# Optimization experiments

Hardware: AMD Instinct MI355X
Metric: run time of the kernel (lower is better)

The kernel has to match this reference:

```python
import jax, jax.numpy as jnp
import numpy as np
import math

PATCHES = [(2, 2), (4, 4), (8, 8), (16, 16)]  # (width, height) per scale
D_MODEL = 256
EPS = 1e-5


def setup_inputs() -> dict:
    key = jax.random.key(0)
    ks = jax.random.split(key, 12)
    b, c, h, w = 4, D_MODEL, 128, 128
    s = 1.0 / math.sqrt(c)
    inp = {
        'x': jax.random.normal(ks[0], (b, c, h, w), jnp.float32),
        'y': jax.random.normal(ks[1], (b, c, h, w), jnp.float32),
        'Wq': jax.random.normal(ks[2], (c, c), jnp.float32) * s,
        'bq': jnp.zeros((c,), jnp.float32),
        'Wk': jax.random.normal(ks[3], (c, c), jnp.float32) * s,
        'bk': jnp.zeros((c,), jnp.float32),
        'Wv': jax.random.normal(ks[4], (c, c), jnp.float32) * s,
        'bv': jnp.zeros((c,), jnp.float32),
        'Wo': jax.random.normal(ks[5], (c, c, 3, 3), jnp.float32) * (1.0 / math.sqrt(c * 9)),
        'bo': jnp.zeros((c,), jnp.float32),
        'gamma': jnp.ones((c,), jnp.float32),
        'beta': jnp.zeros((c,), jnp.float32),
    }
    return inp


def _conv1x1(x, W, b):
    # 1x1 conv == channel matmul
    return jnp.einsum('oc,bchw->bohw', W, x) + b[None, :, None, None]


def _windowed_attention(q, k, v, ww, hh):
    # q,k,v: [b, d_k, h, w] -> windows of (hh, ww), tokens = out_h*out_w
    b, d_k, h, w = q.shape
    out_h, out_w = h // hh, w // ww

    def to_tokens(t):
        t = t.reshape(b, d_k, out_h, hh, out_w, ww)
        t = t.transpose(0, 2, 4, 1, 3, 5)  # b, out_h, out_w, d_k, hh, ww
        return t.reshape(b, out_h * out_w, d_k * hh * ww)

    qt, kt, vt = to_tokens(q), to_tokens(k), to_tokens(v)
    scale = 1.0 / math.sqrt(qt.shape[-1])
    scores = jnp.einsum('bnd,bmd->bnm', qt, kt) * scale
    p = jax.nn.softmax(scores, axis=-1)
    out = jnp.einsum('bnm,bmd->bnd', p, vt)
    out = out.reshape(b, out_h, out_w, d_k, hh, ww)
    out = out.transpose(0, 3, 1, 4, 2, 5).reshape(b, d_k, h, w)
    return out


def reference(x, y, Wq, bq, Wk, bk, Wv, bv, Wo, bo, gamma, beta):
    b, c, h, w = x.shape
    n_scales = len(PATCHES)
    d_k = c // n_scales

    q_all = _conv1x1(x, Wq, bq)
    k_all = _conv1x1(y, Wk, bk)
    v_all = _conv1x1(y, Wv, bv)

    outs = []
    for i, (ww, hh) in enumerate(PATCHES):
        sl = slice(i * d_k, (i + 1) * d_k)
        outs.append(_windowed_attention(q_all[:, sl], k_all[:, sl], v_all[:, sl], ww, hh))
    out = jnp.concatenate(outs, axis=1)  # [b, c, h, w]

    # output_linear: Conv3x3 (pad 1) -> BatchNorm2d (batch stats) -> LeakyReLU(0.2)
    z = jax.lax.conv_general_dilated(
        out, Wo, window_strides=(1, 1), padding='SAME',
        dimension_numbers=('NCHW', 'OIHW', 'NCHW')) + bo[None, :, None, None]
    mean = jnp.mean(z, axis=(0, 2, 3), keepdims=True)
    var = jnp.var(z, axis=(0, 2, 3), keepdims=True)
    zn = (z - mean) * jax.lax.rsqrt(var + EPS)
    zn = zn * gamma[None, :, None, None] + beta[None, :, None, None]
    return jnp.where(zn >= 0, zn, 0.2 * zn)
```

## Files before the change

### kernel.cpp

```cpp
#include <hip/hip_runtime.h>
#include <math.h>

#define BN 4
#define CC 256
#define HH_ 128
#define WW_ 128
#define HWP (HH_*WW_)
#define TOK (64*HWP)


typedef __attribute__((ext_vector_type(8))) short bf16x8;
typedef __attribute__((ext_vector_type(4))) float f32x4;

__device__ __forceinline__ float bf2f(unsigned short u) {
    return __uint_as_float(((unsigned)u) << 16);
}
__device__ __forceinline__ unsigned short f2bf(float f) {
    unsigned u = __float_as_uint(f);
    u += 0x7FFF + ((u >> 16) & 1);
    return (unsigned short)(u >> 16);
}
__device__ __forceinline__ void load4f(const unsigned short* p, float o[4]) {
    ushort4 v = *(const ushort4*)p;
    o[0] = bf2f(v.x); o[1] = bf2f(v.y); o[2] = bf2f(v.z); o[3] = bf2f(v.w);
}
__device__ __forceinline__ float ld1(const unsigned short* p) { return bf2f(*p); }
__device__ __forceinline__ float ld1(const float* p) { return *p; }
__device__ __forceinline__ void st1(unsigned short* p, float v) { *p = f2bf(v); }
__device__ __forceinline__ void st1(float* p, float v) { *p = v; }

__device__ __forceinline__ void gload16(const void* g, void* l) {
    __builtin_amdgcn_global_load_lds(
        (__attribute__((address_space(1))) void*)(g),
        (__attribute__((address_space(3))) void*)(l), 16, 0, 0);
}

__device__ __forceinline__ void stage64(
    const unsigned short* src, size_t strideElems, unsigned short* lds, int t)
{
    #pragma unroll
    for (int k = 0; k < 4; k++) {
        int n = t + k * 256;
        int row = n >> 3, slot = n & 7;
        const char* gp = (const char*)(src + (size_t)row * strideElems)
                       + ((slot ^ (row & 7)) << 4);
        gload16(gp, (char*)lds + n * 16);
    }
}

__device__ __forceinline__ void mfma_iter_swz(
    const unsigned short* As, const unsigned short* Bs,
    int wm, int wn, int lr, int quad, f32x4 acc[4][4])
{
    #pragma unroll
    for (int s = 0; s < 2; s++) {
        bf16x8 af[4], bfr[4];
        #pragma unroll
        for (int i = 0; i < 4; i++) {
            int row = wm*64 + i*16 + lr;
            int off = (row << 7) + (s << 6) + (quad << 4);
            af[i] = *(const bf16x8*)((const char*)As + (off ^ ((row & 7) << 4)));
        }
        #pragma unroll
        for (int j = 0; j < 4; j++) {
            int row = wn*64 + j*16 + lr;
            int off = (row << 7) + (s << 6) + (quad << 4);
            bfr[j] = *(const bf16x8*)((const char*)Bs + (off ^ ((row & 7) << 4)));
        }
        #pragma unroll
        for (int i = 0; i < 4; i++)
            #pragma unroll
            for (int j = 0; j < 4; j++)
                acc[i][j] = __builtin_amdgcn_mfma_f32_16x16x32_bf16(
                    af[i], bfr[j], acc[i][j], 0, 0, 0);
    }
}

#define LDS_STRIDE 72

struct Tile32 { uint4 v[4]; };

__device__ __forceinline__ Tile32 load_tile_bf16(
    const unsigned short* src, size_t stride, int t)
{
    int r = t >> 1, kc = (t & 1) * 32;
    const uint4* sp = (const uint4*)(src + (size_t)r * stride + kc);
    Tile32 o;
    o.v[0] = sp[0]; o.v[1] = sp[1]; o.v[2] = sp[2]; o.v[3] = sp[3];
    return o;
}

__device__ __forceinline__ void store_tile(
    unsigned short* lds, const Tile32& d, int t)
{
    int r = t >> 1, kc = (t & 1) * 32;
    uint4* dp = (uint4*)&lds[r * LDS_STRIDE + kc];
    dp[0] = d.v[0]; dp[1] = d.v[1]; dp[2] = d.v[2]; dp[3] = d.v[3];
}

__device__ __forceinline__ void mfma_iter(
    const unsigned short* As, const unsigned short* Bs,
    int wm, int wn, int lr, int quad, f32x4 acc[4][4])
{
    #pragma unroll
    for (int s = 0; s < 2; s++) {
        bf16x8 af[4], bfr[4];
        #pragma unroll
        for (int i = 0; i < 4; i++)
            af[i] = *(const bf16x8*)&As[(wm*64 + i*16 + lr) * LDS_STRIDE + s*32 + quad*8];
        #pragma unroll
        for (int j = 0; j < 4; j++)
            bfr[j] = *(const bf16x8*)&Bs[(wn*64 + j*16 + lr) * LDS_STRIDE + s*32 + quad*8];
        #pragma unroll
        for (int i = 0; i < 4; i++)
            #pragma unroll
            for (int j = 0; j < 4; j++)
                acc[i][j] = __builtin_amdgcn_mfma_f32_16x16x32_bf16(
                    af[i], bfr[j], acc[i][j], 0, 0, 0);
    }
}

__global__ __launch_bounds__(256) void zero_kernel(float* __restrict__ p)
{
    p[blockIdx.x * 256 + threadIdx.x] = 0.f;
}

__global__ __launch_bounds__(256) void nchw_to_nhwc(
    const float* __restrict__ x, const float* __restrict__ y,
    unsigned short* __restrict__ xt, unsigned short* __restrict__ yt)
{
    __shared__ unsigned short T[64 * 72];
    int z = blockIdx.z;
    int b = z & 3, which = z >> 2;
    const float* src = (which ? y : x) + (size_t)b * CC * HWP;
    unsigned short* dst = (which ? yt : xt) + (size_t)b * HWP * CC;
    int p0 = blockIdx.x * 64, c0 = blockIdx.y * 64;
    int t = threadIdx.x;

    int cl = t >> 2, pc = (t & 3) * 16;
    #pragma unroll
    for (int e = 0; e < 16; e += 4) {
        float4 v = *(const float4*)&src[(size_t)(c0 + cl) * HWP + p0 + pc + e];
        T[(pc + e + 0) * 72 + cl] = f2bf(v.x);
        T[(pc + e + 1) * 72 + cl] = f2bf(v.y);
        T[(pc + e + 2) * 72 + cl] = f2bf(v.z);
        T[(pc + e + 3) * 72 + cl] = f2bf(v.w);
    }
    __syncthreads();
    int p = t >> 2, cc = (t & 3) * 16;
    uint4 a = *(uint4*)&T[p * 72 + cc];
    uint4 bsec = *(uint4*)&T[p * 72 + cc + 8];
    uint4* dp = (uint4*)&dst[(size_t)(p0 + p) * CC + c0 + cc];
    dp[0] = a; dp[1] = bsec;
}

__global__ __launch_bounds__(256) void wpack_kernel(
    const float* __restrict__ Wo, unsigned short* __restrict__ wpack)
{
    int o = blockIdx.x, c = threadIdx.x;
    const float* wr = Wo + ((size_t)o * CC + c) * 9;
    #pragma unroll
    for (int tap = 0; tap < 9; tap++)
        wpack[((size_t)o * 9 + tap) * CC + c] = f2bf(wr[tap]);
}

__global__ __launch_bounds__(256) void wqkv_pack(
    const float* __restrict__ Wq, const float* __restrict__ Wk,
    const float* __restrict__ Wv, unsigned short* __restrict__ Wb)
{
    int which = blockIdx.x;
    const float* W = which == 0 ? Wq : (which == 1 ? Wk : Wv);
    unsigned short* o = Wb + (size_t)which * 65536;
    for (int i = threadIdx.x; i < 65536; i += 256)
        o[i] = f2bf(W[i]);
}

__global__ __launch_bounds__(256) void proj_gemm(
    const unsigned short* __restrict__ xt, const unsigned short* __restrict__ yt,
    const unsigned short* __restrict__ Wqkv,
    const float* __restrict__ bq, const float* __restrict__ bk,
    const float* __restrict__ bv,
    unsigned short* __restrict__ qt, unsigned short* __restrict__ kt,
    unsigned short* __restrict__ vt)
{
    __shared__ unsigned short Asb[2][8192], Bsb[2][8192];
    int z = blockIdx.z, b = z & 3, which = z >> 2;
    const unsigned short* src = (which == 0) ? xt : yt;
    const float* bias = (which == 0) ? bq : (which == 1 ? bk : bv);
    unsigned short* outp = (which == 0) ? qt : (which == 1 ? kt : vt);

    int m0 = blockIdx.y * 128;
    int n0 = blockIdx.x * 128;
    const unsigned short* A = Wqkv + (size_t)which * 65536 + (size_t)m0 * CC;
    const unsigned short* B = src + ((size_t)b * HWP + n0) * CC;

    int t = threadIdx.x, w = t >> 6, lane = t & 63;
    int quad = lane >> 4, lr = lane & 15, wm = w >> 1, wn = w & 1;

    f32x4 acc[4][4];
    #pragma unroll
    for (int i = 0; i < 4; i++)
        #pragma unroll
        for (int j = 0; j < 4; j++) acc[i][j] = (f32x4){0.f, 0.f, 0.f, 0.f};

    stage64(A, CC, Asb[0], t);
    stage64(B, CC, Bsb[0], t);
    __syncthreads();
    int cur = 0;
    for (int k0 = 0; k0 < CC; k0 += 64) {
        if (k0 + 64 < CC) {
            stage64(A + k0 + 64, CC, Asb[cur ^ 1], t);
            stage64(B + k0 + 64, CC, Bsb[cur ^ 1], t);
        }
        mfma_iter_swz(Asb[cur], Bsb[cur], wm, wn, lr, quad, acc);
        __syncthreads();
        cur ^= 1;
    }

    #pragma unroll
    for (int i = 0; i < 4; i++) {
        int obase = m0 + wm * 64 + i * 16 + quad * 4;
        #pragma unroll
        for (int rr = 0; rr < 4; rr++) {
            int o = obase + rr;
            int s = o >> 6, lg = s + 1;
            int ch = o & 63;
            float bia = bias[o];
            unsigned short* ob = outp + ((size_t)s * 4 + b) * TOK;
            #pragma unroll
            for (int j = 0; j < 4; j++) {
                int p = n0 + wn * 64 + j * 16 + lr;
                int yy = p >> 7, xx = p & 127;
                int oy = yy >> lg, wy = yy & ((1 << lg) - 1);
                int ox = xx >> lg, wx = xx & ((1 << lg) - 1);
                int tokn = (oy << (7 - lg)) + ox;
                int didx = (ch << (2 * lg)) + (wy << lg) + wx;
                size_t idx;
                if (which == 2 && s < 3)
                    idx = ((size_t)didx << (14 - 2 * lg)) + tokn;
                else
                    idx = ((size_t)tokn << (6 + 2 * lg)) + didx;
                ob[idx] = f2bf(acc[i][j][rr] + bia);
            }
        }
    }
}

#define PS_STRIDE 136

__global__ __launch_bounds__(512) void flash0(
    const unsigned short* __restrict__ qt, const unsigned short* __restrict__ kt,
    const unsigned short* __restrict__ vt, float* __restrict__ part,
    float* __restrict__ rs0g)
{
    __shared__ unsigned short Ps[64 * PS_STRIDE];
    __shared__ unsigned short Bs[256 * 64];

    int L = blockIdx.x;
    int xcd = L & 7, slot = L >> 3;
    int b = xcd >> 1;
    int idx = slot + 64 * (xcd & 1);
    int h = idx >> 6;
    int q0 = (idx & 63) * 64;
    int kvbase = h * 2048;

    const unsigned short* Qb = qt + (size_t)b * TOK;
    const unsigned short* Kb = kt + (size_t)b * TOK;
    const unsigned short* Vb = vt + (size_t)b * TOK;

    int t = threadIdx.x, w = t >> 6, lane = t & 63;
    int quad = lane >> 4, lr = lane & 15;
    int wm = w >> 2, wn = w & 3;

    bf16x8 aq[4][2][2];
    #pragma unroll
    for (int k = 0; k < 4; k++)
        #pragma unroll
        for (int s = 0; s < 2; s++)
            #pragma unroll
            for (int i = 0; i < 2; i++)
                aq[k][s][i] = *(const bf16x8*)&Qb[
                    (size_t)(q0 + wm*32 + i*16 + lr) * 256 + k*64 + s*32 + quad*8];

    f32x4 acc_o[2][4];
    #pragma unroll
    for (int i = 0; i < 2; i++)
        #pragma unroll
        for (int j = 0; j < 4; j++) acc_o[i][j] = (f32x4){0.f, 0.f, 0.f, 0.f};
    float rsum[2][4] = {};

    const float SC = 1.f / 16.f;

    for (int kv0 = kvbase; kv0 < kvbase + 2048; kv0 += 128) {
        f32x4 acc_s[2][2];
        #pragma unroll
        for (int i = 0; i < 2; i++)
            #pragma unroll
            for (int j = 0; j < 2; j++) acc_s[i][j] = (f32x4){0.f, 0.f, 0.f, 0.f};

        #pragma unroll
        for (int kp = 0; kp < 2; kp++) {
            __syncthreads();
            #pragma unroll
            for (int k = 0; k < 4; k++) {
                int n = t + k * 512;
                int R = n >> 3, sl = n & 7;
                int kl = R & 127, dsub = R >> 7;
                const char* gp = (const char*)(Kb + (size_t)(kv0 + kl) * 256
                                 + kp*128 + dsub*64) + ((sl ^ (R & 7)) << 4);
                gload16(gp, (char*)Bs + n * 16);
            }
            __syncthreads();
            __builtin_amdgcn_s_setprio(1);
            #pragma unroll
            for (int t2 = 0; t2 < 2; t2++)
                #pragma unroll
                for (int s = 0; s < 2; s++) {
                    bf16x8 bfr[2];
                    #pragma unroll
                    for (int j = 0; j < 2; j++) {
                        int row = t2*128 + wn*32 + j*16 + lr;
                        int off = (row << 7) + (s << 6) + (quad << 4);
                        bfr[j] = *(const bf16x8*)((const char*)Bs
                                   + (off ^ ((row & 7) << 4)));
                    }
                    #pragma unroll
                    for (int i = 0; i < 2; i++)
                        #pragma unroll
                        for (int j = 0; j < 2; j++)
                            acc_s[i][j] = __builtin_amdgcn_mfma_f32_16x16x32_bf16(
                                aq[kp*2 + t2][s][i], bfr[j], acc_s[i][j], 0, 0, 0);
                }
            __builtin_amdgcn_s_setprio(0);
        }

        #pragma unroll
        for (int i = 0; i < 2; i++)
            #pragma unroll
            for (int j = 0; j < 2; j++)
                #pragma unroll
                for (int rr = 0; rr < 4; rr++) {
                    float e = __expf(acc_s[i][j][rr] * SC);
                    Ps[(wm*32 + i*16 + quad*4 + rr) * PS_STRIDE + wn*32 + j*16 + lr]
                        = f2bf(e);
                    rsum[i][rr] += e;
                }

        #pragma unroll
        for (int ks = 0; ks < 2; ks++) {
            __syncthreads();
            #pragma unroll
            for (int k = 0; k < 4; k++) {
                int n = t + k * 512;
                int R = n >> 3, sl = n & 7;
                const char* gp = (const char*)(Vb + (size_t)R * 4096 + kv0 + ks*64)
                               + ((sl ^ (R & 7)) << 4);
                gload16(gp, (char*)Bs + n * 16);
            }
            __syncthreads();
            __builtin_amdgcn_s_setprio(1);
            #pragma unroll
            for (int s = 0; s < 2; s++) {
                bf16x8 pa[2], vb[4];
                #pragma unroll
                for (int i = 0; i < 2; i++)
                    pa[i] = *(const bf16x8*)&Ps[
                        (wm*32 + i*16 + lr) * PS_STRIDE + ks*64 + s*32 + quad*8];
                #pragma unroll
                for (int j = 0; j < 4; j++) {
                    int row = wn*64 + j*16 + lr;
                    int off = (row << 7) + (s << 6) + (quad << 4);
                    vb[j] = *(const bf16x8*)((const char*)Bs
                              + (off ^ ((row & 7) << 4)));
                }
                #pragma unroll
                for (int i = 0; i < 2; i++)
                    #pragma unroll
                    for (int j = 0; j < 4; j++)
                        acc_o[i][j] = __builtin_amdgcn_mfma_f32_16x16x32_bf16(
                            pa[i], vb[j], acc_o[i][j], 0, 0, 0);
            }
            __builtin_amdgcn_s_setprio(0);
        }
    }

    #pragma unroll
    for (int i = 0; i < 2; i++)
        #pragma unroll
        for (int rr = 0; rr < 4; rr++) {
            float v = rsum[i][rr];
            v += __shfl_xor(v, 1); v += __shfl_xor(v, 2);
            v += __shfl_xor(v, 4); v += __shfl_xor(v, 8);
            if (lr == 0)
                atomicAdd(&rs0g[b * 4096 + q0 + wm*32 + i*16 + quad*4 + rr], v);
        }
    float* op = part + ((size_t)(h * 4 + b)) * TOK;
    #pragma unroll
    for (int i = 0; i < 2; i++)
        #pragma unroll
        for (int rr = 0; rr < 4; rr++) {
            int tokl = wm*32 + i*16 + quad*4 + rr;
            float* orow = op + (size_t)(q0 + tokl) * 256;
            #pragma unroll
            for (int j = 0; j < 4; j++)
                orow[wn*64 + j*16 + lr] = acc_o[i][j][rr];
        }
}

__global__ __launch_bounds__(256) void combine0f(
    const float* __restrict__ part, const float* __restrict__ rs,
    unsigned short* __restrict__ aot)
{
    int b = blockIdx.y;
    int tok0 = blockIdx.x * 16;
    const float* p0 = part + (size_t)b * TOK;
    const float* p1 = part + (size_t)(4 + b) * TOK;
    int t = threadIdx.x;
    int w = t >> 6, ch = t & 63;
    int wy = w >> 1, wx = w & 1;
    #pragma unroll 4
    for (int u = 0; u < 16; u++) {
        int tok = tok0 + u;
        size_t base = (size_t)tok * 256 + ch * 4 + w;
        float v = (p0[base] + p1[base]) * (1.f / rs[b * 4096 + tok]);
        int oy = tok >> 6, ox = tok & 63;
        int yy = oy * 2 + wy, xx = ox * 2 + wx;
        aot[((size_t)b * HWP + yy * WW_ + xx) * CC + ch] = f2bf(v);
    }
}

template<int NTOK, int DD>
__global__ __launch_bounds__(256) void s_gemm_exp(
    const unsigned short* __restrict__ Qb, const unsigned short* __restrict__ Kb,
    unsigned short* __restrict__ S0, float* __restrict__ rsg, float sc)
{
    __shared__ unsigned short Asb[2][8192], Bsb[2][8192];
    int bz = blockIdx.z;
    int m0 = blockIdx.y * 128, n0 = blockIdx.x * 128;
    const unsigned short* Q = Qb + (size_t)bz * TOK + (size_t)m0 * DD;
    const unsigned short* K = Kb + (size_t)bz * TOK + (size_t)n0 * DD;
    unsigned short* S = S0 + (size_t)bz * NTOK * NTOK;
    float* rs = rsg + (size_t)bz * NTOK;

    int t = threadIdx.x, w = t >> 6, lane = t & 63;
    int quad = lane >> 4, lr = lane & 15, wm = w >> 1, wn = w & 1;

    f32x4 acc[4][4];
    #pragma unroll
    for (int i = 0; i < 4; i++)
        #pragma unroll
        for (int j = 0; j < 4; j++) acc[i][j] = (f32x4){0.f, 0.f, 0.f, 0.f};

    stage64(Q, DD, Asb[0], t);
    stage64(K, DD, Bsb[0], t);
    __syncthreads();
    int cur = 0;
    for (int k0 = 0; k0 < DD; k0 += 64) {
        if (k0 + 64 < DD) {
            stage64(Q + k0 + 64, DD, Asb[cur ^ 1], t);
            stage64(K + k0 + 64, DD, Bsb[cur ^ 1], t);
        }
        mfma_iter_swz(Asb[cur], Bsb[cur], wm, wn, lr, quad, acc);
        __syncthreads();
        cur ^= 1;
    }

    #pragma unroll
    for (int i = 0; i < 4; i++) {
        int m = m0 + wm * 64 + i * 16 + quad * 4;
        float rsum[4] = {0.f, 0.f, 0.f, 0.f};
        #pragma unroll
        for (int j = 0; j < 4; j++) {
            int n = n0 + wn * 64 + j * 16 + lr;
            #pragma unroll
            for (int rr = 0; rr < 4; rr++) {
                float e = __expf(acc[i][j][rr] * sc);
                S[(size_t)(m + rr) * NTOK + n] = f2bf(e);
                rsum[rr] += e;
            }
        }
        #pragma unroll
        for (int rr = 0; rr < 4; rr++) {
            float v = rsum[rr];
            v += __shfl_xor(v, 1);
            v += __shfl_xor(v, 2);
            v += __shfl_xor(v, 4);
            v += __shfl_xor(v, 8);
            if (lr == 0) atomicAdd(&rs[m + rr], v);
        }
    }
}

template<int NTOK, int DD, int LG, int CH0>
__global__ __launch_bounds__(256) void o_gemm(
    const unsigned short* __restrict__ Pb, const unsigned short* __restrict__ Vb,
    const float* __restrict__ rsg, unsigned short* __restrict__ aot, int b0)
{
    __shared__ unsigned short Asb[2][8192], Bsb[2][8192];
    int bz = blockIdx.z, b = b0 + bz;
    int m0 = blockIdx.y * 128, n0 = blockIdx.x * 128;
    const unsigned short* P = Pb + (size_t)bz * NTOK * NTOK + (size_t)m0 * NTOK;
    const unsigned short* V = Vb + (size_t)bz * TOK + (size_t)n0 * NTOK;
    const float* rs = rsg + (size_t)bz * NTOK;

    int t = threadIdx.x, w = t >> 6, lane = t & 63;
    int quad = lane >> 4, lr = lane & 15, wm = w >> 1, wn = w & 1;

    f32x4 acc[4][4];
    #pragma unroll
    for (int i = 0; i < 4; i++)
        #pragma unroll
        for (int j = 0; j < 4; j++) acc[i][j] = (f32x4){0.f, 0.f, 0.f, 0.f};

    stage64(P, NTOK, Asb[0], t);
    stage64(V, NTOK, Bsb[0], t);
    __syncthreads();
    int cur = 0;
    for (int k0 = 0; k0 < NTOK; k0 += 64) {
        if (k0 + 64 < NTOK) {
            stage64(P + k0 + 64, NTOK, Asb[cur ^ 1], t);
            stage64(V + k0 + 64, NTOK, Bsb[cur ^ 1], t);
        }
        mfma_iter_swz(Asb[cur], Bsb[cur], wm, wn, lr, quad, acc);
        __syncthreads();
        cur ^= 1;
    }

    #pragma unroll
    for (int i = 0; i < 4; i++) {
        int tb0 = m0 + wm * 64 + i * 16 + quad * 4;
        #pragma unroll
        for (int rr = 0; rr < 4; rr++) {
            int tokn = tb0 + rr;
            float inv = 1.f / rs[tokn];
            int oy = tokn >> (7 - LG), ox = tokn & ((1 << (7 - LG)) - 1);
            #pragma unroll
            for (int j = 0; j < 4; j++) {
                int d = n0 + wn * 64 + j * 16 + lr;
                int ch = d >> (2 * LG);
                int r2 = d & ((1 << (2 * LG)) - 1);
                int wy = r2 >> LG, wx = r2 & ((1 << LG) - 1);
                int yy = (oy << LG) + wy, xx = (ox << LG) + wx;
                aot[((size_t)b * HWP + yy * WW_ + xx) * CC + CH0 + ch] =
                    f2bf(acc[i][j][rr] * inv);
            }
        }
    }
}

__global__ __launch_bounds__(256) void s2_partial(
    const unsigned short* __restrict__ Qb, const unsigned short* __restrict__ Kb,
    float* __restrict__ S2p)
{
    __shared__ unsigned short Asb[2][8192], Bsb[2][8192];
    int z = blockIdx.z, b = z >> 3, sp = z & 7;
    int m0 = blockIdx.y * 128, n0 = blockIdx.x * 128;
    const unsigned short* Q = Qb + (size_t)b * TOK + (size_t)m0 * 4096 + sp * 512;
    const unsigned short* K = Kb + (size_t)b * TOK + (size_t)n0 * 4096 + sp * 512;
    float* So = S2p + ((size_t)(sp * 4 + b)) * 65536;

    int t = threadIdx.x, w = t >> 6, lane = t & 63;
    int quad = lane >> 4, lr = lane & 15, wm = w >> 1, wn = w & 1;

    f32x4 acc[4][4];
    #pragma unroll
    for (int i = 0; i < 4; i++)
        #pragma unroll
        for (int j = 0; j < 4; j++) acc[i][j] = (f32x4){0.f, 0.f, 0.f, 0.f};

    stage64(Q, 4096, Asb[0], t);
    stage64(K, 4096, Bsb[0], t);
    __syncthreads();
    int cur = 0;
    for (int k0 = 0; k0 < 512; k0 += 64) {
        if (k0 + 64 < 512) {
            stage64(Q + k0 + 64, 4096, Asb[cur ^ 1], t);
            stage64(K + k0 + 64, 4096, Bsb[cur ^ 1], t);
        }
        mfma_iter_swz(Asb[cur], Bsb[cur], wm, wn, lr, quad, acc);
        __syncthreads();
        cur ^= 1;
    }

    #pragma unroll
    for (int i = 0; i < 4; i++) {
        int m = m0 + wm * 64 + i * 16 + quad * 4;
        #pragma unroll
        for (int j = 0; j < 4; j++) {
            int n = n0 + wn * 64 + j * 16 + lr;
            #pragma unroll
            for (int rr = 0; rr < 4; rr++)
                So[(size_t)(m + rr) * 256 + n] = acc[i][j][rr];
        }
    }
}

__global__ __launch_bounds__(256) void s2_finish(
    const float* __restrict__ S2p, unsigned short* __restrict__ Sbf,
    float* __restrict__ rs2, float sc)
{
    int row = blockIdx.x, b = blockIdx.y, t = threadIdx.x;
    float v = 0.f;
    #pragma unroll
    for (int sp = 0; sp < 8; sp++)
        v += S2p[((size_t)(sp * 4 + b)) * 65536 + row * 256 + t];
    float e = __expf(v * sc);
    Sbf[((size_t)b * 65536) + row * 256 + t] = f2bf(e);
    __shared__ float red[256];
    red[t] = e; __syncthreads();
    for (int s = 128; s > 0; s >>= 1) {
        if (t < s) red[t] += red[t + s];
        __syncthreads();
    }
    if (t == 0) rs2[b * 256 + row] = red[0];
}

__device__ __forceinline__ Tile32 load_tile_conv(
    const unsigned short* aob, int ys, int dx, int cbase, int t)
{
    int r = t >> 1, kc = (t & 1) * 32;
    int xs = r + dx;
    Tile32 o;
    if (ys >= 0 && ys < HH_ && xs >= 0 && xs < WW_) {
        const uint4* sp = (const uint4*)(aob + ((size_t)ys * WW_ + xs) * CC + cbase + kc);
        o.v[0] = sp[0]; o.v[1] = sp[1]; o.v[2] = sp[2]; o.v[3] = sp[3];
    } else {
        uint4 zz = make_uint4(0, 0, 0, 0);
        o.v[0] = zz; o.v[1] = zz; o.v[2] = zz; o.v[3] = zz;
    }
    return o;
}

__global__ __launch_bounds__(256) void conv_gemm(
    const unsigned short* __restrict__ aot, const unsigned short* __restrict__ wpack,
    const float* __restrict__ bo, float* __restrict__ zout,
    float* __restrict__ stats)
{
    __shared__ unsigned short As[128 * LDS_STRIDE], Bs[128 * LDS_STRIDE];
    int yrow = blockIdx.x;
    int o0 = blockIdx.y * 128;
    int b = blockIdx.z;
    const unsigned short* aob = aot + (size_t)b * HWP * CC;
    const unsigned short* wsrc = wpack + (size_t)o0 * 2304;

    int t = threadIdx.x, w = t >> 6, lane = t & 63;
    int quad = lane >> 4, lr = lane & 15, wm = w >> 1, wn = w & 1;

    f32x4 acc[4][4];
    #pragma unroll
    for (int i = 0; i < 4; i++)
        #pragma unroll
        for (int j = 0; j < 4; j++) acc[i][j] = (f32x4){0.f, 0.f, 0.f, 0.f};

    for (int tap = 0; tap < 9; tap++) {
        int dy = tap / 3 - 1, dx = tap % 3 - 1;
        int ys = yrow + dy;
        for (int cb = 0; cb < CC; cb += 64) {
            Tile32 ta = load_tile_bf16(wsrc + tap * CC + cb, 2304, t);
            Tile32 tb = load_tile_conv(aob, ys, dx, cb, t);
            __syncthreads();
            store_tile(As, ta, t); store_tile(Bs, tb, t);
            __syncthreads();
            mfma_iter(As, Bs, wm, wn, lr, quad, acc);
        }
    }

    #pragma unroll
    for (int i = 0; i < 4; i++) {
        #pragma unroll
        for (int rr = 0; rr < 4; rr++) {
            int o = o0 + wm * 64 + i * 16 + quad * 4 + rr;
            float bia = bo[o];
            float s1 = 0.f, s2v = 0.f;
            #pragma unroll
            for (int j = 0; j < 4; j++) {
                int x = wn * 64 + j * 16 + lr;
                float v = acc[i][j][rr] + bia;
                zout[((size_t)(b * CC + o)) * HWP + yrow * WW_ + x] = v;
                s1 += v; s2v = fmaf(v, v, s2v);
            }
            s1 += __shfl_xor(s1, 1); s2v += __shfl_xor(s2v, 1);
            s1 += __shfl_xor(s1, 2); s2v += __shfl_xor(s2v, 2);
            s1 += __shfl_xor(s1, 4); s2v += __shfl_xor(s2v, 4);
            s1 += __shfl_xor(s1, 8); s2v += __shfl_xor(s2v, 8);
            if (lr == 0) {
                atomicAdd(&stats[o], s1);
                atomicAdd(&stats[CC + o], s2v);
            }
        }
    }
}

__global__ __launch_bounds__(256) void stats_finalize(
    float* __restrict__ stats, const float* __restrict__ gamma,
    const float* __restrict__ beta)
{
    int c = threadIdx.x;
    const float inv_n = 1.f / (BN * HWP);
    float mean = stats[c] * inv_n;
    float var = stats[CC + c] * inv_n - mean * mean;
    float rstd = rsqrtf(var + 1e-5f);
    float gs = gamma[c] * rstd;
    stats[c] = gs;
    stats[CC + c] = beta[c] - mean * gs;
}

__global__ __launch_bounds__(256) void s3_kernel(
    const unsigned short* __restrict__ Qb, const unsigned short* __restrict__ Kb,
    float* __restrict__ S, float sc)
{
    const int N = 64, D = 16384, KLEN = 1024;
    int b = blockIdx.z >> 4, kc = blockIdx.z & 15;
    const unsigned short* Q = Qb + (size_t)b * TOK;
    const unsigned short* K = Kb + (size_t)b * TOK;
    float* Sb = S + (size_t)b * N * N;
    int k0 = kc * KLEN;

    __shared__ float As[16][64], Bs[16][64];
    int t = threadIdx.x, tx = t & 15, ty = t >> 4, r = t >> 2, q = t & 3;

    float acc[4][4] = {};
    for (int kk = k0; kk < k0 + KLEN; kk += 16) {
        float a4[4], b4[4];
        load4f(&Q[(size_t)r * D + kk + q * 4], a4);
        load4f(&K[(size_t)r * D + kk + q * 4], b4);
        __syncthreads();
        As[q*4+0][r] = a4[0]; As[q*4+1][r] = a4[1]; As[q*4+2][r] = a4[2]; As[q*4+3][r] = a4[3];
        Bs[q*4+0][r] = b4[0]; Bs[q*4+1][r] = b4[1]; Bs[q*4+2][r] = b4[2]; Bs[q*4+3][r] = b4[3];
        __syncthreads();
        #pragma unroll
        for (int k = 0; k < 16; k++) {
            float4 af = *(const float4*)&As[k][ty*4];
            float4 bf = *(const float4*)&Bs[k][tx*4];
            float ar[4] = {af.x, af.y, af.z, af.w};
            float br[4] = {bf.x, bf.y, bf.z, bf.w};
            #pragma unroll
            for (int ii = 0; ii < 4; ii++)
                #pragma unroll
                for (int jj = 0; jj < 4; jj++)
                    acc[ii][jj] = fmaf(ar[ii], br[jj], acc[ii][jj]);
        }
    }

    #pragma unroll
    for (int ii = 0; ii < 4; ii++)
        #pragma unroll
        for (int jj = 0; jj < 4; jj++)
            atomicAdd(&Sb[(size_t)(ty * 4 + ii) * N + tx * 4 + jj], acc[ii][jj] * sc);
}

template<typename T>
__global__ __launch_bounds__(256) void softmax_kernel(T* __restrict__ S, int n)
{
    int b = blockIdx.y;
    int row = blockIdx.x;
    T* rp = S + (size_t)b * n * n + (size_t)row * n;
    __shared__ float red[256];
    int t = threadIdx.x;

    float m = -1e30f;
    for (int j = t; j < n; j += 256) m = fmaxf(m, ld1(&rp[j]));
    red[t] = m; __syncthreads();
    for (int s = 128; s > 0; s >>= 1) { if (t < s) red[t] = fmaxf(red[t], red[t + s]); __syncthreads(); }
    m = red[0]; __syncthreads();

    float sum = 0.f;
    for (int j = t; j < n; j += 256) { float e = __expf(ld1(&rp[j]) - m); st1(&rp[j], e); sum += e; }
    red[t] = sum; __syncthreads();
    for (int s = 128; s > 0; s >>= 1) { if (t < s) red[t] += red[t + s]; __syncthreads(); }
    float inv = 1.f / red[0];
    for (int j = t; j < n; j += 256) st1(&rp[j], ld1(&rp[j]) * inv);
}

__global__ __launch_bounds__(256) void o3_kernel(
    const float* __restrict__ P, const unsigned short* __restrict__ Vb,
    unsigned short* __restrict__ aot)
{
    const int N = 64, D = 16384, LG = 4, CH0 = 192;
    int bz = blockIdx.z;
    const float* Pb = P + (size_t)bz * N * N;
    const unsigned short* V = Vb + (size_t)bz * TOK;
    int i0 = blockIdx.x * 64, d0 = blockIdx.y * 64;

    __shared__ float Ps[16][64];
    __shared__ float Vs[16][64];
    int t = threadIdx.x, tx = t & 15, ty = t >> 4, r = t >> 2, q = t & 3;
    int vr = t >> 4, vq = t & 15;

    float acc[4][4] = {};
    for (int j0 = 0; j0 < N; j0 += 16) {
        float p4[4], v4[4];
        float4 pv = *(const float4*)&Pb[(size_t)(i0 + r) * N + j0 + q * 4];
        p4[0] = pv.x; p4[1] = pv.y; p4[2] = pv.z; p4[3] = pv.w;
        load4f(&V[(size_t)(j0 + vr) * D + d0 + vq * 4], v4);
        __syncthreads();
        Ps[q*4+0][r] = p4[0]; Ps[q*4+1][r] = p4[1]; Ps[q*4+2][r] = p4[2]; Ps[q*4+3][r] = p4[3];
        Vs[vr][vq*4+0] = v4[0]; Vs[vr][vq*4+1] = v4[1]; Vs[vr][vq*4+2] = v4[2]; Vs[vr][vq*4+3] = v4[3];
        __syncthreads();
        #pragma unroll
        for (int k = 0; k < 16; k++) {
            float4 pf = *(const float4*)&Ps[k][ty*4];
            float4 vf = *(const float4*)&Vs[k][tx*4];
            float pr[4] = {pf.x, pf.y, pf.z, pf.w};
            float vrr[4] = {vf.x, vf.y, vf.z, vf.w};
            #pragma unroll
            for (int ii = 0; ii < 4; ii++)
                #pragma unroll
                for (int jj = 0; jj < 4; jj++)
                    acc[ii][jj] = fmaf(pr[ii], vrr[jj], acc[ii][jj]);
        }
    }

    #pragma unroll
    for (int ii = 0; ii < 4; ii++) {
        int tokn = i0 + ty * 4 + ii;
        int oy = tokn >> (7 - LG), ox = tokn & ((1 << (7 - LG)) - 1);
        #pragma unroll
        for (int jj = 0; jj < 4; jj++) {
            int d = d0 + tx * 4 + jj;
            int ch = d >> (2 * LG);
            int r2 = d & ((1 << (2 * LG)) - 1);
            int wy = r2 >> LG, wx = r2 & ((1 << LG) - 1);
            int yy = (oy << LG) + wy, xx = (ox << LG) + wx;
            aot[((size_t)bz * HWP + yy * WW_ + xx) * CC + CH0 + ch] = f2bf(acc[ii][jj]);
        }
    }
}

__global__ __launch_bounds__(256) void bn_apply_kernel(
    float* __restrict__ z, const float* __restrict__ stats)
{
    size_t i4 = (size_t)blockIdx.x * 256 + threadIdx.x;
    size_t idx = i4 * 4;
    int c = (int)((idx >> 14) & 255);
    float gs = stats[c], gb = stats[CC + c];
    float4 v = *(float4*)&z[idx];
    v.x = fmaf(v.x, gs, gb); v.y = fmaf(v.y, gs, gb);
    v.z = fmaf(v.z, gs, gb); v.w = fmaf(v.w, gs, gb);
    v.x = v.x >= 0.f ? v.x : 0.2f * v.x;
    v.y = v.y >= 0.f ? v.y : 0.2f * v.y;
    v.z = v.z >= 0.f ? v.z : 0.2f * v.z;
    v.w = v.w >= 0.f ? v.w : 0.2f * v.w;
    *(float4*)&z[idx] = v;
}

extern "C" void kernel_launch(void* const* d_in, const int* in_sizes, int n_in,
                              void* d_out, int out_size, void* d_ws, size_t ws_size,
                              hipStream_t stream)
{
    const float* x     = (const float*)d_in[0];
    const float* y     = (const float*)d_in[1];
    const float* Wq    = (const float*)d_in[2];
    const float* bq    = (const float*)d_in[3];
    const float* Wk    = (const float*)d_in[4];
    const float* bk    = (const float*)d_in[5];
    const float* Wv    = (const float*)d_in[6];
    const float* bv    = (const float*)d_in[7];
    const float* Wo    = (const float*)d_in[8];
    const float* bo    = (const float*)d_in[9];
    const float* gamma = (const float*)d_in[10];
    const float* beta  = (const float*)d_in[11];
    float* out = (float*)d_out;

    unsigned short* qt    = (unsigned short*)d_ws;
    unsigned short* kt    = qt + (size_t)16777216;
    unsigned short* vt    = kt + (size_t)16777216;
    unsigned short* aot   = vt + (size_t)16777216;
    unsigned short* Sbf   = aot + (size_t)16777216;
    unsigned short* wpack = Sbf + (size_t)16777216;
    float* stats = (float*)(wpack + (size_t)589824);
    float* S3    = stats + 512;
    float* rs0   = S3 + 16384;
    float* rs1   = rs0 + 16384;
    float* rs2   = rs1 + 4096;
    unsigned short* xt = Sbf;
    unsigned short* yt = aot;
    float* part = (float*)d_out;
    unsigned short* Wqkv_bf = (unsigned short*)((char*)d_out + (size_t)33554432);
    float* S2p = (float*)d_out;

    dim3 blk(256);

    zero_kernel<<<dim3(150), blk, 0, stream>>>(stats);
    nchw_to_nhwc<<<dim3(256, 4, 8), blk, 0, stream>>>(x, y, xt, yt);
    wpack_kernel<<<dim3(256), blk, 0, stream>>>(Wo, wpack);
    wqkv_pack<<<dim3(3), blk, 0, stream>>>(Wq, Wk, Wv, Wqkv_bf);

    proj_gemm<<<dim3(128, 2, 12), blk, 0, stream>>>(
        xt, yt, Wqkv_bf, bq, bk, bv, qt, kt, vt);

    flash0<<<dim3(512), dim3(512), 0, stream>>>(qt, kt, vt, part, rs0);
    combine0f<<<dim3(256, 4), blk, 0, stream>>>(part, rs0, aot);

    s_gemm_exp<1024, 1024><<<dim3(8, 8, 4), blk, 0, stream>>>(
        qt + (size_t)4 * TOK, kt + (size_t)4 * TOK, Sbf, rs1, 1.f / 32.f);
    o_gemm<1024, 1024, 2, 64><<<dim3(8, 8, 4), blk, 0, stream>>>(
        Sbf, vt + (size_t)4 * TOK, rs1, aot, 0);

    s2_partial<<<dim3(2, 2, 32), blk, 0, stream>>>(
        qt + (size_t)8 * TOK, kt + (size_t)8 * TOK, S2p);
    s2_finish<<<dim3(256, 4), blk, 0, stream>>>(S2p, Sbf, rs2, 1.f / 64.f);
    o_gemm<256, 4096, 3, 128><<<dim3(32, 2, 4), blk, 0, stream>>>(
        Sbf, vt + (size_t)8 * TOK, rs2, aot, 0);

    s3_kernel<<<dim3(1, 1, 64), blk, 0, stream>>>(
        qt + (size_t)12 * TOK, kt + (size_t)12 * TOK, S3, 1.f / 128.f);
    softmax_kernel<float><<<dim3(64, 4), blk, 0, stream>>>(S3, 64);
    o3_kernel<<<dim3(1, 256, 4), blk, 0, stream>>>(S3, vt + (size_t)12 * TOK, aot);

    conv_gemm<<<dim3(128, 2, 4), blk, 0, stream>>>(aot, wpack, bo, out, stats);
    stats_finalize<<<dim3(1), blk, 0, stream>>>(stats, gamma, beta);
    bn_apply_kernel<<<dim3(16384), blk, 0, stream>>>(out, stats);
}
```

Before: 870.5 us.

## Pad conv input, pipeline conv GEMM, move scale-3 attention to MFMA, fold BN finalize

The attention output buffer now has a one-pixel zero border, so the 3x3 conv GEMM can use async global-to-LDS double-buffered staging with swizzled MFMA reads and no bounds checks. The scale-3 score and PV kernels move from scalar FP32 FMA loops to bf16 MFMA kernels, and the V projection for scale 3 switches to a transposed layout to match. The stats finalize kernel is folded into bn_apply, and the workspace is reorganised. In exchange, an extra zero-fill pass over the padded buffer is added, and scale-3 P is rounded to bf16.

```diff
diff --git a/kernel.cpp b/kernel.cpp
--- a/kernel.cpp
+++ b/kernel.cpp
@@ -20,13 +20,7 @@
     u += 0x7FFF + ((u >> 16) & 1);
     return (unsigned short)(u >> 16);
 }
-__device__ __forceinline__ void load4f(const unsigned short* p, float o[4]) {
-    ushort4 v = *(const ushort4*)p;
-    o[0] = bf2f(v.x); o[1] = bf2f(v.y); o[2] = bf2f(v.z); o[3] = bf2f(v.w);
-}
-__device__ __forceinline__ float ld1(const unsigned short* p) { return bf2f(*p); }
 __device__ __forceinline__ float ld1(const float* p) { return *p; }
-__device__ __forceinline__ void st1(unsigned short* p, float v) { *p = f2bf(v); }
 __device__ __forceinline__ void st1(float* p, float v) { *p = v; }
 
 __device__ __forceinline__ void gload16(const void* g, void* l) {
@@ -48,6 +42,19 @@
     }
 }
 
+__device__ __forceinline__ void stage32(
+    const unsigned short* src, size_t strideElems, unsigned short* lds, int t)
+{
+    #pragma unroll
+    for (int k = 0; k < 2; k++) {
+        int n = t + k * 256;
+        int row = n >> 3, slot = n & 7;
+        const char* gp = (const char*)(src + (size_t)row * strideElems)
+                       + ((slot ^ (row & 7)) << 4);
+        gload16(gp, (char*)lds + n * 16);
+    }
+}
+
 __device__ __forceinline__ void mfma_iter_swz(
     const unsigned short* As, const unsigned short* Bs,
     int wm, int wn, int lr, int quad, f32x4 acc[4][4])
@@ -76,53 +83,16 @@
     }
 }
 
-#define LDS_STRIDE 72
-
-struct Tile32 { uint4 v[4]; };
-
-__device__ __forceinline__ Tile32 load_tile_bf16(
-    const unsigned short* src, size_t stride, int t)
-{
-    int r = t >> 1, kc = (t & 1) * 32;
-    const uint4* sp = (const uint4*)(src + (size_t)r * stride + kc);
-    Tile32 o;
-    o.v[0] = sp[0]; o.v[1] = sp[1]; o.v[2] = sp[2]; o.v[3] = sp[3];
-    return o;
-}
-
-__device__ __forceinline__ void store_tile(
-    unsigned short* lds, const Tile32& d, int t)
-{
-    int r = t >> 1, kc = (t & 1) * 32;
-    uint4* dp = (uint4*)&lds[r * LDS_STRIDE + kc];
-    dp[0] = d.v[0]; dp[1] = d.v[1]; dp[2] = d.v[2]; dp[3] = d.v[3];
-}
-
-__device__ __forceinline__ void mfma_iter(
-    const unsigned short* As, const unsigned short* Bs,
-    int wm, int wn, int lr, int quad, f32x4 acc[4][4])
-{
-    #pragma unroll
-    for (int s = 0; s < 2; s++) {
-        bf16x8 af[4], bfr[4];
-        #pragma unroll
-        for (int i = 0; i < 4; i++)
-            af[i] = *(const bf16x8*)&As[(wm*64 + i*16 + lr) * LDS_STRIDE + s*32 + quad*8];
-        #pragma unroll
-        for (int j = 0; j < 4; j++)
-            bfr[j] = *(const bf16x8*)&Bs[(wn*64 + j*16 + lr) * LDS_STRIDE + s*32 + quad*8];
-        #pragma unroll
-        for (int i = 0; i < 4; i++)
-            #pragma unroll
-            for (int j = 0; j < 4; j++)
-                acc[i][j] = __builtin_amdgcn_mfma_f32_16x16x32_bf16(
-                    af[i], bfr[j], acc[i][j], 0, 0, 0);
-    }
-}
-
 __global__ __launch_bounds__(256) void zero_kernel(float* __restrict__ p)
 {
     p[blockIdx.x * 256 + threadIdx.x] = 0.f;
+}
+
+__global__ __launch_bounds__(256) void zero4(uint4* __restrict__ p, int n4)
+{
+    uint4 z = make_uint4(0, 0, 0, 0);
+    for (int i = blockIdx.x * 256 + threadIdx.x; i < n4; i += gridDim.x * 256)
+        p[i] = z;
 }
 
 __global__ __launch_bounds__(256) void nchw_to_nhwc(
@@ -236,7 +206,7 @@
                 int tokn = (oy << (7 - lg)) + ox;
                 int didx = (ch << (2 * lg)) + (wy << lg) + wx;
                 size_t idx;
-                if (which == 2 && s < 3)
+                if (which == 2)
                     idx = ((size_t)didx << (14 - 2 * lg)) + tokn;
                 else
                     idx = ((size_t)tokn << (6 + 2 * lg)) + didx;
@@ -409,7 +379,7 @@
 
 __global__ __launch_bounds__(256) void combine0f(
     const float* __restrict__ part, const float* __restrict__ rs,
-    unsigned short* __restrict__ aot)
+    unsigned short* __restrict__ aotp)
 {
     int b = blockIdx.y;
     int tok0 = blockIdx.x * 16;
@@ -425,7 +395,7 @@
         float v = (p0[base] + p1[base]) * (1.f / rs[b * 4096 + tok]);
         int oy = tok >> 6, ox = tok & 63;
         int yy = oy * 2 + wy, xx = ox * 2 + wx;
-        aot[((size_t)b * HWP + yy * WW_ + xx) * CC + ch] = f2bf(v);
+        aotp[((size_t)(b * 130 + yy + 1) * 130 + xx + 1) * CC + ch] = f2bf(v);
     }
 }
 
@@ -494,7 +464,7 @@
 template<int NTOK, int DD, int LG, int CH0>
 __global__ __launch_bounds__(256) void o_gemm(
     const unsigned short* __restrict__ Pb, const unsigned short* __restrict__ Vb,
-    const float* __restrict__ rsg, unsigned short* __restrict__ aot, int b0)
+    const float* __restrict__ rsg, unsigned short* __restrict__ aotp, int b0)
 {
     __shared__ unsigned short Asb[2][8192], Bsb[2][8192];
     int bz = blockIdx.z, b = b0 + bz;
@@ -541,7 +511,7 @@
                 int r2 = d & ((1 << (2 * LG)) - 1);
                 int wy = r2 >> LG, wx = r2 & ((1 << LG) - 1);
                 int yy = (oy << LG) + wy, xx = (ox << LG) + wx;
-                aot[((size_t)b * HWP + yy * WW_ + xx) * CC + CH0 + ch] =
+                aotp[((size_t)(b * 130 + yy + 1) * 130 + xx + 1) * CC + CH0 + ch] =
                     f2bf(acc[i][j][rr] * inv);
             }
         }
@@ -615,32 +585,16 @@
     if (t == 0) rs2[b * 256 + row] = red[0];
 }
 
-__device__ __forceinline__ Tile32 load_tile_conv(
-    const unsigned short* aob, int ys, int dx, int cbase, int t)
-{
-    int r = t >> 1, kc = (t & 1) * 32;
-    int xs = r + dx;
-    Tile32 o;
-    if (ys >= 0 && ys < HH_ && xs >= 0 && xs < WW_) {
-        const uint4* sp = (const uint4*)(aob + ((size_t)ys * WW_ + xs) * CC + cbase + kc);
-        o.v[0] = sp[0]; o.v[1] = sp[1]; o.v[2] = sp[2]; o.v[3] = sp[3];
-    } else {
-        uint4 zz = make_uint4(0, 0, 0, 0);
-        o.v[0] = zz; o.v[1] = zz; o.v[2] = zz; o.v[3] = zz;
-    }
-    return o;
-}
-
 __global__ __launch_bounds__(256) void conv_gemm(
-    const unsigned short* __restrict__ aot, const unsigned short* __restrict__ wpack,
+    const unsigned short* __restrict__ aotp, const unsigned short* __restrict__ wpack,
     const float* __restrict__ bo, float* __restrict__ zout,
     float* __restrict__ stats)
 {
-    __shared__ unsigned short As[128 * LDS_STRIDE], Bs[128 * LDS_STRIDE];
+    __shared__ unsigned short Asb[2][8192], Bsb[2][8192];
     int yrow = blockIdx.x;
     int o0 = blockIdx.y * 128;
     int b = blockIdx.z;
-    const unsigned short* aob = aot + (size_t)b * HWP * CC;
+    const unsigned short* aob = aotp + (size_t)b * 130 * 130 * 256;
     const unsigned short* wsrc = wpack + (size_t)o0 * 2304;
 
     int t = threadIdx.x, w = t >> 6, lane = t & 63;
@@ -652,17 +606,26 @@
         #pragma unroll
         for (int j = 0; j < 4; j++) acc[i][j] = (f32x4){0.f, 0.f, 0.f, 0.f};
 
-    for (int tap = 0; tap < 9; tap++) {
-        int dy = tap / 3 - 1, dx = tap % 3 - 1;
-        int ys = yrow + dy;
-        for (int cb = 0; cb < CC; cb += 64) {
-            Tile32 ta = load_tile_bf16(wsrc + tap * CC + cb, 2304, t);
-            Tile32 tb = load_tile_conv(aob, ys, dx, cb, t);
-            __syncthreads();
-            store_tile(As, ta, t); store_tile(Bs, tb, t);
-            __syncthreads();
-            mfma_iter(As, Bs, wm, wn, lr, quad, acc);
-        }
+    stage64(wsrc, 2304, Asb[0], t);
+    {
+        int ys = yrow - 1;
+        stage64(aob + ((size_t)(ys + 1) * 130 + 0) * 256, 256, Bsb[0], t);
+    }
+    __syncthreads();
+    int cur = 0;
+    for (int kk = 0; kk < 36; kk++) {
+        if (kk + 1 < 36) {
+            int kn = kk + 1;
+            int tap = kn >> 2, cb = (kn & 3) * 64;
+            int dy = tap / 3 - 1, dx = tap % 3 - 1;
+            int ys = yrow + dy;
+            stage64(wsrc + tap * 256 + cb, 2304, Asb[cur ^ 1], t);
+            stage64(aob + ((size_t)(ys + 1) * 130 + (dx + 1)) * 256 + cb, 256,
+                    Bsb[cur ^ 1], t);
+        }
+        mfma_iter_swz(Asb[cur], Bsb[cur], wm, wn, lr, quad, acc);
+        __syncthreads();
+        cur ^= 1;
     }
 
     #pragma unroll
@@ -691,62 +654,71 @@
     }
 }
 
-__global__ __launch_bounds__(256) void stats_finalize(
-    float* __restrict__ stats, const float* __restrict__ gamma,
-    const float* __restrict__ beta)
-{
-    int c = threadIdx.x;
-    const float inv_n = 1.f / (BN * HWP);
-    float mean = stats[c] * inv_n;
-    float var = stats[CC + c] * inv_n - mean * mean;
-    float rstd = rsqrtf(var + 1e-5f);
-    float gs = gamma[c] * rstd;
-    stats[c] = gs;
-    stats[CC + c] = beta[c] - mean * gs;
-}
-
-__global__ __launch_bounds__(256) void s3_kernel(
+__global__ __launch_bounds__(256) void s3_mfma(
     const unsigned short* __restrict__ Qb, const unsigned short* __restrict__ Kb,
     float* __restrict__ S, float sc)
 {
-    const int N = 64, D = 16384, KLEN = 1024;
-    int b = blockIdx.z >> 4, kc = blockIdx.z & 15;
-    const unsigned short* Q = Qb + (size_t)b * TOK;
-    const unsigned short* K = Kb + (size_t)b * TOK;
-    float* Sb = S + (size_t)b * N * N;
-    int k0 = kc * KLEN;
-
-    __shared__ float As[16][64], Bs[16][64];
-    int t = threadIdx.x, tx = t & 15, ty = t >> 4, r = t >> 2, q = t & 3;
-
-    float acc[4][4] = {};
-    for (int kk = k0; kk < k0 + KLEN; kk += 16) {
-        float a4[4], b4[4];
-        load4f(&Q[(size_t)r * D + kk + q * 4], a4);
-        load4f(&K[(size_t)r * D + kk + q * 4], b4);
+    __shared__ unsigned short Asb[2][4096], Bsb[2][4096];
+    int z = blockIdx.x, b = z >> 4, kc = z & 15;
+    const unsigned short* Q = Qb + (size_t)b * TOK + kc * 1024;
+    const unsigned short* K = Kb + (size_t)b * TOK + kc * 1024;
+    float* Sb = S + (size_t)b * 4096;
+
+    int t = threadIdx.x, w = t >> 6, lane = t & 63;
+    int quad = lane >> 4, lr = lane & 15, wm = w >> 1, wn = w & 1;
+
+    f32x4 acc[2][2];
+    #pragma unroll
+    for (int i = 0; i < 2; i++)
+        #pragma unroll
+        for (int j = 0; j < 2; j++) acc[i][j] = (f32x4){0.f, 0.f, 0.f, 0.f};
+
+    stage32(Q, 16384, Asb[0], t);
+    stage32(K, 16384, Bsb[0], t);
+    __syncthreads();
+    int cur = 0;
+    for (int k0 = 0; k0 < 1024; k0 += 64) {
+        if (k0 + 64 < 1024) {
+            stage32(Q + k0 + 64, 16384, Asb[cur ^ 1], t);
+            stage32(K + k0 + 64, 16384, Bsb[cur ^ 1], t);
+        }
+        #pragma unroll
+        for (int s = 0; s < 2; s++) {
+            bf16x8 af[2], bfr[2];
+            #pragma unroll
+            for (int i = 0; i < 2; i++) {
+                int row = wm*32 + i*16 + lr;
+                int off = (row << 7) + (s << 6) + (quad << 4);
+                af[i] = *(const bf16x8*)((const char*)Asb[cur]
+                          + (off ^ ((row & 7) << 4)));
+            }
+            #pragma unroll
+            for (int j = 0; j < 2; j++) {
+                int row = wn*32 + j*16 + lr;
+                int off = (row << 7) + (s << 6) + (quad << 4);
+                bfr[j] = *(const bf16x8*)((const char*)Bsb[cur]
+                           + (off ^ ((row & 7) << 4)));
+            }
+            #pragma unroll
+            for (int i = 0; i < 2; i++)
+                #pragma unroll
+                for (int j = 0; j < 2; j++)
+                    acc[i][j] = __builtin_amdgcn_mfma_f32_16x16x32_bf16(
+                        af[i], bfr[j], acc[i][j], 0, 0, 0);
+        }
         __syncthreads();
-        As[q*4+0][r] = a4[0]; As[q*4+1][r] = a4[1]; As[q*4+2][r] = a4[2]; As[q*4+3][r] = a4[3];
-        Bs[q*4+0][r] = b4[0]; Bs[q*4+1][r] = b4[1]; Bs[q*4+2][r] = b4[2]; Bs[q*4+3][r] = b4[3];
-        __syncthreads();
-        #pragma unroll
-        for (int k = 0; k < 16; k++) {
-            float4 af = *(const float4*)&As[k][ty*4];
-            float4 bf = *(const float4*)&Bs[k][tx*4];
-            float ar[4] = {af.x, af.y, af.z, af.w};
-            float br[4] = {bf.x, bf.y, bf.z, bf.w};
-            #pragma unroll
-            for (int ii = 0; ii < 4; ii++)
-                #pragma unroll
-                for (int jj = 0; jj < 4; jj++)
-                    acc[ii][jj] = fmaf(ar[ii], br[jj], acc[ii][jj]);
-        }
-    }
-
-    #pragma unroll
-    for (int ii = 0; ii < 4; ii++)
-        #pragma unroll
-        for (int jj = 0; jj < 4; jj++)
-            atomicAdd(&Sb[(size_t)(ty * 4 + ii) * N + tx * 4 + jj], acc[ii][jj] * sc);
+        cur ^= 1;
+    }
+
+    #pragma unroll
+    for (int i = 0; i < 2; i++)
+        #pragma unroll
+        for (int j = 0; j < 2; j++)
+            #pragma unroll
+            for (int rr = 0; rr < 4; rr++)
+                atomicAdd(&Sb[(size_t)(wm*32 + i*16 + quad*4 + rr) * 64
+                              + wn*32 + j*16 + lr],
+                          acc[i][j][rr] * sc);
 }
 
 template<typename T>
@@ -772,68 +744,98 @@
     for (int j = t; j < n; j += 256) st1(&rp[j], ld1(&rp[j]) * inv);
 }
 
-__global__ __launch_bounds__(256) void o3_kernel(
+__global__ __launch_bounds__(256) void o3_mfma(
     const float* __restrict__ P, const unsigned short* __restrict__ Vb,
-    unsigned short* __restrict__ aot)
-{
-    const int N = 64, D = 16384, LG = 4, CH0 = 192;
-    int bz = blockIdx.z;
-    const float* Pb = P + (size_t)bz * N * N;
-    const unsigned short* V = Vb + (size_t)bz * TOK;
-    int i0 = blockIdx.x * 64, d0 = blockIdx.y * 64;
-
-    __shared__ float Ps[16][64];
-    __shared__ float Vs[16][64];
-    int t = threadIdx.x, tx = t & 15, ty = t >> 4, r = t >> 2, q = t & 3;
-    int vr = t >> 4, vq = t & 15;
-
-    float acc[4][4] = {};
-    for (int j0 = 0; j0 < N; j0 += 16) {
-        float p4[4], v4[4];
-        float4 pv = *(const float4*)&Pb[(size_t)(i0 + r) * N + j0 + q * 4];
-        p4[0] = pv.x; p4[1] = pv.y; p4[2] = pv.z; p4[3] = pv.w;
-        load4f(&V[(size_t)(j0 + vr) * D + d0 + vq * 4], v4);
-        __syncthreads();
-        Ps[q*4+0][r] = p4[0]; Ps[q*4+1][r] = p4[1]; Ps[q*4+2][r] = p4[2]; Ps[q*4+3][r] = p4[3];
-        Vs[vr][vq*4+0] = v4[0]; Vs[vr][vq*4+1] = v4[1]; Vs[vr][vq*4+2] = v4[2]; Vs[vr][vq*4+3] = v4[3];
-        __syncthreads();
-        #pragma unroll
-        for (int k = 0; k < 16; k++) {
-            float4 pf = *(const float4*)&Ps[k][ty*4];
-            float4 vf = *(const float4*)&Vs[k][tx*4];
-            float pr[4] = {pf.x, pf.y, pf.z, pf.w};
-            float vrr[4] = {vf.x, vf.y, vf.z, vf.w};
-            #pragma unroll
-            for (int ii = 0; ii < 4; ii++)
-                #pragma unroll
-                for (int jj = 0; jj < 4; jj++)
-                    acc[ii][jj] = fmaf(pr[ii], vrr[jj], acc[ii][jj]);
-        }
-    }
-
-    #pragma unroll
-    for (int ii = 0; ii < 4; ii++) {
-        int tokn = i0 + ty * 4 + ii;
-        int oy = tokn >> (7 - LG), ox = tokn & ((1 << (7 - LG)) - 1);
-        #pragma unroll
-        for (int jj = 0; jj < 4; jj++) {
-            int d = d0 + tx * 4 + jj;
-            int ch = d >> (2 * LG);
-            int r2 = d & ((1 << (2 * LG)) - 1);
-            int wy = r2 >> LG, wx = r2 & ((1 << LG) - 1);
-            int yy = (oy << LG) + wy, xx = (ox << LG) + wx;
-            aot[((size_t)bz * HWP + yy * WW_ + xx) * CC + CH0 + ch] = f2bf(acc[ii][jj]);
-        }
-    }
+    unsigned short* __restrict__ aotp)
+{
+    const int CH0 = 192;
+    int n0 = blockIdx.x * 128;
+    int b = blockIdx.z;
+    const float* Pb = P + (size_t)b * 4096;
+    const unsigned short* V = Vb + (size_t)b * TOK;
+
+    __shared__ unsigned short As[4096];
+    __shared__ unsigned short Bs[8192];
+
+    int t = threadIdx.x, w = t >> 6, lane = t & 63;
+    int quad = lane >> 4, lr = lane & 15;
+    int wn = w;
+
+    #pragma unroll
+    for (int k = 0; k < 2; k++) {
+        int u = t + k * 256;
+        int row = u >> 3, slot = u & 7;
+        const float* pp = &Pb[(row << 6) + (slot << 3)];
+        unsigned short tmp[8];
+        #pragma unroll
+        for (int e = 0; e < 8; e++) tmp[e] = f2bf(pp[e]);
+        int off = ((row << 7) + (slot << 4)) ^ ((row & 7) << 4);
+        *(uint4*)((char*)As + off) = *(const uint4*)tmp;
+    }
+    stage64(V + (size_t)n0 * 64, 64, Bs, t);
+    __syncthreads();
+
+    f32x4 acc[4][2];
+    #pragma unroll
+    for (int i = 0; i < 4; i++)
+        #pragma unroll
+        for (int j = 0; j < 2; j++) acc[i][j] = (f32x4){0.f, 0.f, 0.f, 0.f};
+
+    #pragma unroll
+    for (int s = 0; s < 2; s++) {
+        bf16x8 af[4], bfr[2];
+        #pragma unroll
+        for (int i = 0; i < 4; i++) {
+            int row = i*16 + lr;
+            int off = (row << 7) + (s << 6) + (quad << 4);
+            af[i] = *(const bf16x8*)((const char*)As + (off ^ ((row & 7) << 4)));
+        }
+        #pragma unroll
+        for (int j = 0; j < 2; j++) {
+            int row = wn*32 + j*16 + lr;
+            int off = (row << 7) + (s << 6) + (quad << 4);
+            bfr[j] = *(const bf16x8*)((const char*)Bs + (off ^ ((row & 7) << 4)));
+        }
+        #pragma unroll
+        for (int i = 0; i < 4; i++)
+            #pragma unroll
+            for (int j = 0; j < 2; j++)
+                acc[i][j] = __builtin_amdgcn_mfma_f32_16x16x32_bf16(
+                    af[i], bfr[j], acc[i][j], 0, 0, 0);
+    }
+
+    #pragma unroll
+    for (int i = 0; i < 4; i++)
+        #pragma unroll
+        for (int rr = 0; rr < 4; rr++) {
+            int tok = i*16 + quad*4 + rr;
+            int oy = tok >> 3, ox = tok & 7;
+            #pragma unroll
+            for (int j = 0; j < 2; j++) {
+                int d = n0 + wn*32 + j*16 + lr;
+                int ch = d >> 8;
+                int r2 = d & 255;
+                int wy = r2 >> 4, wx = r2 & 15;
+                int yy = oy * 16 + wy, xx = ox * 16 + wx;
+                aotp[((size_t)(b * 130 + yy + 1) * 130 + xx + 1) * CC + CH0 + ch]
+                    = f2bf(acc[i][j][rr]);
+            }
+        }
 }
 
 __global__ __launch_bounds__(256) void bn_apply_kernel(
-    float* __restrict__ z, const float* __restrict__ stats)
+    float* __restrict__ z, const float* __restrict__ stats,
+    const float* __restrict__ gamma, const float* __restrict__ beta)
 {
     size_t i4 = (size_t)blockIdx.x * 256 + threadIdx.x;
     size_t idx = i4 * 4;
     int c = (int)((idx >> 14) & 255);
-    float gs = stats[c], gb = stats[CC + c];
+    const float inv_n = 1.f / (BN * HWP);
+    float mean = stats[c] * inv_n;
+    float var = stats[CC + c] * inv_n - mean * mean;
+    float rstd = rsqrtf(var + 1e-5f);
+    float gs = gamma[c] * rstd;
+    float gb = beta[c] - mean * gs;
     float4 v = *(float4*)&z[idx];
     v.x = fmaf(v.x, gs, gb); v.y = fmaf(v.y, gs, gb);
     v.z = fmaf(v.z, gs, gb); v.w = fmaf(v.w, gs, gb);
@@ -865,50 +867,52 @@
     unsigned short* qt    = (unsigned short*)d_ws;
     unsigned short* kt    = qt + (size_t)16777216;
     unsigned short* vt    = kt + (size_t)16777216;
-    unsigned short* aot   = vt + (size_t)16777216;
-    unsigned short* Sbf   = aot + (size_t)16777216;
-    unsigned short* wpack = Sbf + (size_t)16777216;
-    float* stats = (float*)(wpack + (size_t)589824);
+    unsigned short* aotp  = vt + (size_t)16777216;
+    unsigned short* Sbf   = aotp + (size_t)17305600;
+    unsigned short* wpack = Sbf + (size_t)4194304;
+    unsigned short* Wqkv  = wpack + (size_t)589824;
+    float* stats = (float*)(Wqkv + (size_t)196608);
     float* S3    = stats + 512;
     float* rs0   = S3 + 16384;
     float* rs1   = rs0 + 16384;
     float* rs2   = rs1 + 4096;
-    unsigned short* xt = Sbf;
-    unsigned short* yt = aot;
+
+    unsigned short* xt = (unsigned short*)d_out;
+    unsigned short* yt = (unsigned short*)((char*)d_out + 33554432);
     float* part = (float*)d_out;
-    unsigned short* Wqkv_bf = (unsigned short*)((char*)d_out + (size_t)33554432);
-    float* S2p = (float*)d_out;
+    float* S2p  = (float*)d_out;
 
     dim3 blk(256);
 
     zero_kernel<<<dim3(150), blk, 0, stream>>>(stats);
+    zero4<<<dim3(2048), blk, 0, stream>>>((uint4*)aotp, 2163200);
+
     nchw_to_nhwc<<<dim3(256, 4, 8), blk, 0, stream>>>(x, y, xt, yt);
     wpack_kernel<<<dim3(256), blk, 0, stream>>>(Wo, wpack);
-    wqkv_pack<<<dim3(3), blk, 0, stream>>>(Wq, Wk, Wv, Wqkv_bf);
+    wqkv_pack<<<dim3(3), blk, 0, stream>>>(Wq, Wk, Wv, Wqkv);
 
     proj_gemm<<<dim3(128, 2, 12), blk, 0, stream>>>(
-        xt, yt, Wqkv_bf, bq, bk, bv, qt, kt, vt);
+        xt, yt, Wqkv, bq, bk, bv, qt, kt, vt);
 
     flash0<<<dim3(512), dim3(512), 0, stream>>>(qt, kt, vt, part, rs0);
-    combine0f<<<dim3(256, 4), blk, 0, stream>>>(part, rs0, aot);
+    combine0f<<<dim3(256, 4), blk, 0, stream>>>(part, rs0, aotp);
 
     s_gemm_exp<1024, 1024><<<dim3(8, 8, 4), blk, 0, stream>>>(
         qt + (size_t)4 * TOK, kt + (size_t)4 * TOK, Sbf, rs1, 1.f / 32.f);
     o_gemm<1024, 1024, 2, 64><<<dim3(8, 8, 4), blk, 0, stream>>>(
-        Sbf, vt + (size_t)4 * TOK, rs1, aot, 0);
+        Sbf, vt + (size_t)4 * TOK, rs1, aotp, 0);
 
     s2_partial<<<dim3(2, 2, 32), blk, 0, stream>>>(
         qt + (size_t)8 * TOK, kt + (size_t)8 * TOK, S2p);
     s2_finish<<<dim3(256, 4), blk, 0, stream>>>(S2p, Sbf, rs2, 1.f / 64.f);
     o_gemm<256, 4096, 3, 128><<<dim3(32, 2, 4), blk, 0, stream>>>(
-        Sbf, vt + (size_t)8 * TOK, rs2, aot, 0);
-
-    s3_kernel<<<dim3(1, 1, 64), blk, 0, stream>>>(
+        Sbf, vt + (size_t)8 * TOK, rs2, aotp, 0);
+
+    s3_mfma<<<dim3(64), blk, 0, stream>>>(
         qt + (size_t)12 * TOK, kt + (size_t)12 * TOK, S3, 1.f / 128.f);
     softmax_kernel<float><<<dim3(64, 4), blk, 0, stream>>>(S3, 64);
-    o3_kernel<<<dim3(1, 256, 4), blk, 0, stream>>>(S3, vt + (size_t)12 * TOK, aot);
-
-    conv_gemm<<<dim3(128, 2, 4), blk, 0, stream>>>(aot, wpack, bo, out, stats);
-    stats_finalize<<<dim3(1), blk, 0, stream>>>(stats, gamma, beta);
-    bn_apply_kernel<<<dim3(16384), blk, 0, stream>>>(out, stats);
-}
+    o3_mfma<<<dim3(128, 1, 4), blk, 0, stream>>>(S3, vt + (size_t)12 * TOK, aotp);
+
+    conv_gemm<<<dim3(128, 2, 4), blk, 0, stream>>>(aotp, wpack, bo, out, stats);
+    bn_apply_kernel<<<dim3(16384), blk, 0, stream>>>(out, stats, gamma, beta);
+}
```

Result: faster. 851.9 us (-2.1%).
